# Kernel tuning notes

Measured on AMD Instinct MI355X. Metric: run time of the kernel, lower is better.

## Reference

```python
import jax, jax.numpy as jnp
import numpy as np

B, LQ, LF, NW, NFR, E, D, V = 4, 128, 64, 2, 8, 128, 128, 64


def _project(x, W, b):
    # torch Emb_Projection('linear'): Linear then zero-row mask
    y = x @ W + b
    m = 1.0 - jnp.all(y == 0, axis=-1, keepdims=True).astype(y.dtype)
    return y * m


def setup_inputs() -> dict:
    key = jax.random.key(0)
    ks = jax.random.split(key, 12)
    s = lambda k, shape, fan: jax.random.normal(k, shape, jnp.float32) / np.sqrt(fan)
    return {
        "query": jax.random.normal(ks[0], (B, LQ, E), jnp.float32),
        "fragment": jax.random.normal(ks[1], (B, NW, NFR, LF, E), jnp.float32),
        "query_mask": jnp.ones((B, LQ), jnp.float32),
        "fragment_mask": jnp.ones((B, NW, NFR, LF), jnp.float32),
        # learned params (stored [in, out]; torch Linear is x @ W.T with W [out,in])
        "proj_W": s(ks[2], (E, D), E),
        "proj_b": jnp.zeros((D,), jnp.float32),
        "self_att_W": s(ks[3], (NW, D), D),   # n_way Linear(D,1,bias=False)
        "q_att_W": s(ks[4], (D, V), D),
        "f_att_W": s(ks[5], (D, V), D),
        "qf_att_W": s(ks[6], (D, V), D),
        "gate_w": s(ks[7], (V,), V),          # value_gate: Linear(V,1,bias=False)
        "val_w": s(ks[8], (V,), V),           # value_att:  Linear(V,1,bias=False)
    }


def reference(query, fragment, query_mask, fragment_mask, proj_W, proj_b,
              self_att_W, q_att_W, f_att_W, qf_att_W, gate_w, val_w):
    query = _project(query, proj_W, proj_b)          # [B,Lq,D]
    fragment = _project(fragment, proj_W, proj_b)    # [B,NW,NFR,Lf,D]

    # (1) fragment self-attention -> frag_code
    logits = jnp.einsum('bwfld,wd->bwfl', fragment, self_att_W)   # per-way Linear(D,1)
    e = jnp.exp(logits) * fragment_mask
    frag_self_att = e / (e.sum(-1, keepdims=True) + 1e-7)          # [B,NW,NFR,Lf]
    frag_code = (fragment * frag_self_att[..., None]).sum(-2)     # [B,NW,NFR,D]

    # (2) query-to-fragment attention
    frag_r = fragment.reshape(fragment.shape[0], -1, fragment.shape[-2], fragment.shape[-1])  # [B,NF,Lf,D]
    qr = query[:, None]                                            # [B,1,Lq,D]
    q_att = qr @ q_att_W                                           # [B,1,Lq,V]
    f_att = frag_r @ f_att_W                                       # [B,NF,Lf,V]
    # large broadcast product [B,NF,Lf,Lq,D] then project to V
    qf = (qr[:, :, None, :, :] * frag_r[:, :, :, None, :]) @ qf_att_W  # [B,NF,Lf,Lq,V]
    qf = q_att[:, :, None] + f_att[:, :, :, None] + qf
    qf = qf.max(axis=-3)                                           # max over Lf -> [B,NF,Lq,V]

    qf_gate = jax.nn.sigmoid(qf @ gate_w) * query_mask[:, None]    # [B,NF,Lq]
    e2 = jnp.exp(qf @ val_w) * query_mask[:, None]
    qf_norm = e2 / (e2.sum(-1, keepdims=True) + 1e-7)              # [B,NF,Lq]

    query_code = (qr * qf_norm[..., None]).sum(axis=2)             # [B,NF,D]
    query_code = query_code.reshape(frag_code.shape)               # [B,NW,NFR,D]
    return frag_code, query_code, frag_self_att, qf_gate, query
```

## Files before the change

### kernel.cpp

```cpp
#include <hip/hip_runtime.h>
#include <hip/hip_bf16.h>

#define B_   4
#define LQ_  128
#define LF_  64
#define NW_  2
#define NFR_ 8
#define E_   128
#define D_   128
#define V_   64
#define NWF_ (NW_*NFR_)

using bf16 = __hip_bfloat16;
typedef unsigned short u16;
typedef unsigned int   u32;
typedef __attribute__((ext_vector_type(8))) short  bf16x8;
typedef __attribute__((ext_vector_type(2))) float  f32x2;
typedef __attribute__((ext_vector_type(4))) float  f32x4;
typedef __attribute__((ext_vector_type(4))) u32    u32x4;

#define WS_PWT   0
#define WS_QAT   8192
#define WS_W3T   12288
#define WS_WFT   16384
#define WS_E2    20480
#define WS_QPB   28672

#define OUT_FRAGCODE  0
#define OUT_QUERYCODE 8192
#define OUT_SELFATT   16384
#define OUT_QFGATE    20480
#define OUT_QUERY     28672

#define L_FP   0
#define L_QP   16384
#define L_FA   24576
#define L_QAT  33792
#define L_SAW  38400
#define L_ATT  38912
#define L_RED  39168
#define L_PM   41216
#define L_TOT  57600

__device__ __forceinline__ float us2f(u16 v) { return __uint_as_float((u32)v << 16); }
__device__ __forceinline__ float lo2f(u32 v) { return __uint_as_float(v << 16); }
__device__ __forceinline__ float hi2f(u32 v) { return __uint_as_float(v & 0xffff0000u); }
__device__ __forceinline__ u16 f2b_raw(float f) {
    u32 u = __float_as_uint(f);
    return (u16)((u + 0x7fffu + ((u >> 16) & 1u)) >> 16);
}
__device__ __forceinline__ u32 pk2(float hi, float lo) {
    return __builtin_amdgcn_perm(__float_as_uint(hi), __float_as_uint(lo), 0x07060302u);
}
template<bool BF> __device__ __forceinline__ float LD(const void* p, int i) {
    return BF ? us2f(((const u16*)p)[i]) : ((const float*)p)[i];
}
template<bool BF> __device__ __forceinline__ void ST(void* p, int i, float v) {
    if (BF) ((u16*)p)[i] = f2b_raw(v); else ((float*)p)[i] = v;
}
template<bool BF> __device__ __forceinline__ u16 LDB(const void* p, int i) {
    return BF ? ((const u16*)p)[i] : f2b_raw(((const float*)p)[i]);
}
__device__ __forceinline__ bool is_bf(const void* qmask) {
    return ((const u16*)qmask)[0] == 0x3F80u;
}
template<bool BF>
__device__ __forceinline__ bf16x8 loadA(const void* x, int row, int kt, int quad) {
    int off = row * 128 + kt * 32 + quad * 8;
    if (BF) return *(const bf16x8*)((const u16*)x + off);
    f32x4 a = *(const f32x4*)((const float*)x + off);
    f32x4 c = *(const f32x4*)((const float*)x + off + 4);
    u32x4 av;
    av.x = pk2(a.y, a.x); av.y = pk2(a.w, a.z);
    av.z = pk2(c.y, c.x); av.w = pk2(c.w, c.z);
    return __builtin_bit_cast(bf16x8, av);
}

template<bool BF>
__device__ __forceinline__ void prep_body(const void* src, u16* dst, u16* stg,
                                          int N, int k0)
{
    int t = threadIdx.x, st = N + 1, total = 32 * N;
    for (int i = t; i < total; i += 256) {
        int k = i / N, v = i % N;
        stg[k * st + v] = LDB<BF>(src, (k0 + k) * N + v);
    }
    __syncthreads();
    for (int j = t; j < total; j += 256) {
        int n = j >> 5, kk = j & 31;
        dst[n * 128 + k0 + kk] = stg[kk * st + n];
    }
}
__global__ __launch_bounds__(256) void k_prep(
    const void* projW, const void* qattW, const void* qfW, const void* fattW,
    const void* qmask, float* ws)
{
    __shared__ u16 stg[32 * 129];
    int mat = blockIdx.x >> 2, kq = blockIdx.x & 3;
    const void* src = (mat == 0) ? projW : (mat == 1) ? qattW : (mat == 2) ? qfW : fattW;
    u16* dst = (u16*)(ws + ((mat == 0) ? WS_PWT : (mat == 1) ? WS_QAT : (mat == 2) ? WS_W3T : WS_WFT));
    int N = (mat == 0) ? 128 : 64;
    if (is_bf(qmask)) prep_body<true >(src, dst, stg, N, kq * 32);
    else              prep_body<false>(src, dst, stg, N, kq * 32);
}

template<bool BF>
__device__ __forceinline__ void main_body(
    const void* query, const void* fragment, const void* qmask, const void* fmask,
    const void* projB, const void* saW, const void* gatew, const void* valw,
    float* ws, void* out, char* smem)
{
    u16*   s_fp  = (u16*)(smem + L_FP);
    u16*   s_qp  = (u16*)(smem + L_QP);
    u16*   s_fa  = (u16*)(smem + L_FA);
    u16*   s_qat = (u16*)(smem + L_QAT);
    float* s_saw = (float*)(smem + L_SAW);
    float* s_att = (float*)(smem + L_ATT);
    float* s_red = (float*)(smem + L_RED);
    u16*   s_pm  = (u16*)(smem + L_PM);

    int bx = blockIdx.x;
    int qt = bx >> 6, bwf = bx & 63, b = bwf >> 4;
    int t = threadIdx.x, lane = t & 63, w = t >> 6;
    int m = lane & 15, quad = lane >> 4;
    int sk = (m & 7) << 3;
    const u16* pwt = (const u16*)(ws + WS_PWT);
    const u16* qatw = (const u16*)(ws + WS_QAT);
    const u16* w3t = (const u16*)(ws + WS_W3T);
    const u16* wft = (const u16*)(ws + WS_WFT);
    bool do_fragatt = (qt == (bwf & 3));
    bool do_export  = ((bwf & 15) == 0);

    if (w < 4) {
        bf16x8 afr[4];
        #pragma unroll
        for (int kt = 0; kt < 4; ++kt)
            afr[kt] = loadA<BF>(fragment, bwf * 64 + w * 16 + m, kt, quad);
        #pragma unroll
        for (int nt = 0; nt < 8; ++nt) {
            int n = nt * 16 + m;
            float bv = LD<BF>(projB, n);
            f32x4 acc = (f32x4){bv, bv, bv, bv};
            #pragma unroll
            for (int kt = 0; kt < 4; ++kt) {
                bf16x8 bw = *(const bf16x8*)(pwt + n * 128 + kt * 32 + quad * 8);
                acc = __builtin_amdgcn_mfma_f32_16x16x32_bf16(afr[kt], bw, acc, 0, 0, 0);
            }
            #pragma unroll
            for (int rr = 0; rr < 4; ++rr) {
                int row = w * 16 + quad * 4 + rr;
                s_fp[row * 128 + (n ^ ((row & 7) << 3))] = f2b_raw(acc[rr]);
            }
        }
    } else if (w < 6) {
        int q0 = (w - 4) * 16;
        bf16x8 afq[4];
        #pragma unroll
        for (int kt = 0; kt < 4; ++kt)
            afq[kt] = loadA<BF>(query, b * 128 + qt * 32 + q0 + m, kt, quad);
        #pragma unroll
        for (int nt = 0; nt < 8; ++nt) {
            int n = nt * 16 + m;
            float bv = LD<BF>(projB, n);
            f32x4 acc = (f32x4){bv, bv, bv, bv};
            #pragma unroll
            for (int kt = 0; kt < 4; ++kt) {
                bf16x8 bw = *(const bf16x8*)(pwt + n * 128 + kt * 32 + quad * 8);
                acc = __builtin_amdgcn_mfma_f32_16x16x32_bf16(afq[kt], bw, acc, 0, 0, 0);
            }
            #pragma unroll
            for (int rr = 0; rr < 4; ++rr) {
                int row = q0 + quad * 4 + rr;
                s_qp[row * 128 + (n ^ ((row & 7) << 3))] = f2b_raw(acc[rr]);
            }
        }
    }
    __syncthreads();

    if (w < 4) {
        bf16x8 afa[4];
        #pragma unroll
        for (int kt = 0; kt < 4; ++kt)
            afa[kt] = *(const bf16x8*)&s_fp[(w * 16 + m) * 128 + ((kt * 32 + quad * 8) ^ sk)];
        #pragma unroll
        for (int vt = 0; vt < 4; ++vt) {
            f32x4 a0 = (f32x4){0.f, 0.f, 0.f, 0.f};
            #pragma unroll
            for (int kt = 0; kt < 4; ++kt) {
                bf16x8 wk = *(const bf16x8*)(wft + (vt * 16 + m) * 128 + kt * 32 + quad * 8);
                a0 = __builtin_amdgcn_mfma_f32_16x16x32_bf16(afa[kt], wk, a0, 0, 0, 0);
            }
            #pragma unroll
            for (int r = 0; r < 4; ++r)
                s_fa[(w * 16 + quad * 4 + r) * 72 + vt * 16 + m] = f2b_raw(a0[r]);
        }
    } else if (w < 6) {
        int q0 = (w - 4) * 16;
        bf16x8 aq[4];
        #pragma unroll
        for (int kt = 0; kt < 4; ++kt)
            aq[kt] = *(const bf16x8*)&s_qp[(q0 + m) * 128 + ((kt * 32 + quad * 8) ^ sk)];
        #pragma unroll
        for (int vt = 0; vt < 4; ++vt) {
            f32x4 a0 = (f32x4){0.f, 0.f, 0.f, 0.f};
            #pragma unroll
            for (int kt = 0; kt < 4; ++kt) {
                bf16x8 bk = *(const bf16x8*)(qatw + (vt * 16 + m) * 128 + kt * 32 + quad * 8);
                a0 = __builtin_amdgcn_mfma_f32_16x16x32_bf16(aq[kt], bk, a0, 0, 0, 0);
            }
            #pragma unroll
            for (int r = 0; r < 4; ++r)
                s_qat[(q0 + quad * 4 + r) * 72 + vt * 16 + m] = f2b_raw(a0[r]);
        }
    }
    __syncthreads();

    int qsub = w & 1, lq = w >> 1;
    bf16x8 w3f[4][4];
    #pragma unroll
    for (int vt = 0; vt < 4; ++vt)
        #pragma unroll
        for (int kt = 0; kt < 4; ++kt)
            w3f[vt][kt] = *(const bf16x8*)(w3t + (vt * 16 + m) * 128 + kt * 32 + quad * 8);
    f32x2 qp2[4][4];
    {
        #pragma unroll
        for (int kt = 0; kt < 4; ++kt) {
            bf16x8 aq2 = *(const bf16x8*)&s_qp[(qsub * 16 + m) * 128 + ((kt * 32 + quad * 8) ^ sk)];
            u32x4 uv = __builtin_bit_cast(u32x4, aq2);
            qp2[kt][0] = (f32x2){lo2f(uv.x), hi2f(uv.x)};
            qp2[kt][1] = (f32x2){lo2f(uv.y), hi2f(uv.y)};
            qp2[kt][2] = (f32x2){lo2f(uv.z), hi2f(uv.z)};
            qp2[kt][3] = (f32x2){lo2f(uv.w), hi2f(uv.w)};
        }
    }
    float mx[4][4];
    #pragma unroll
    for (int vt = 0; vt < 4; ++vt)
        #pragma unroll
        for (int r = 0; r < 4; ++r) mx[vt][r] = -1e30f;

    int lbase = lq * 16;
    #pragma unroll 2
    for (int li = 0; li < 16; ++li) {
        int l = lbase + li;
        int sw = (l & 7) << 3;
        bf16x8 af[4];
        #pragma unroll
        for (int kt = 0; kt < 4; ++kt) {
            u32x4 fv = *(const u32x4*)&s_fp[l * 128 + ((kt * 32 + quad * 8) ^ sw)];
            f32x2 p0 = qp2[kt][0] * (f32x2){lo2f(fv.x), hi2f(fv.x)};
            f32x2 p1 = qp2[kt][1] * (f32x2){lo2f(fv.y), hi2f(fv.y)};
            f32x2 p2 = qp2[kt][2] * (f32x2){lo2f(fv.z), hi2f(fv.z)};
            f32x2 p3 = qp2[kt][3] * (f32x2){lo2f(fv.w), hi2f(fv.w)};
            u32x4 av;
            av.x = pk2(p0.y, p0.x);
            av.y = pk2(p1.y, p1.x);
            av.z = pk2(p2.y, p2.x);
            av.w = pk2(p3.y, p3.x);
            af[kt] = __builtin_bit_cast(bf16x8, av);
        }
        #pragma unroll
        for (int vt = 0; vt < 4; ++vt) {
            float fa = us2f(s_fa[l * 72 + vt * 16 + m]);
            f32x4 acc = (f32x4){fa, fa, fa, fa};
            #pragma unroll
            for (int kt = 0; kt < 4; ++kt)
                acc = __builtin_amdgcn_mfma_f32_16x16x32_bf16(af[kt], w3f[vt][kt], acc, 0, 0, 0);
            #pragma unroll
            for (int r = 0; r < 4; ++r) mx[vt][r] = fmaxf(mx[vt][r], acc[r]);
        }
    }
    #pragma unroll
    for (int vt = 0; vt < 4; ++vt)
        #pragma unroll
        for (int r = 0; r < 4; ++r) {
            int q = qsub * 16 + quad * 4 + r;
            s_pm[(lq * 32 + q) * 64 + ((vt * 16 + m) ^ (((q >> 2) & 3) << 4))] = f2b_raw(mx[vt][r]);
        }
    __syncthreads();

    {
        int q = t >> 4, vg = t & 15;
        int gq = qt * 32 + q;
        int swq = ((q >> 2) & 3) << 4;
        float gp = 0.f, ep = 0.f;
        #pragma unroll
        for (int jj = 0; jj < 4; ++jj) {
            int v = vg * 4 + jj;
            int c = v ^ swq;
            float m01 = fmaxf(us2f(s_pm[q * 64 + c]),        us2f(s_pm[(32 + q) * 64 + c]));
            float m23 = fmaxf(us2f(s_pm[(64 + q) * 64 + c]), us2f(s_pm[(96 + q) * 64 + c]));
            float qf = fmaxf(m01, m23) + us2f(s_qat[q * 72 + v]);
            gp += qf * LD<BF>(gatew, v);
            ep += qf * LD<BF>(valw, v);
        }
        #pragma unroll
        for (int off = 1; off <= 8; off <<= 1) {
            gp += __shfl_xor(gp, off, 64);
            ep += __shfl_xor(ep, off, 64);
        }
        if (vg == 0) {
            float qm = LD<BF>(qmask, b * 128 + gq);
            float g = (1.0f / (1.0f + expf(-gp))) * qm;
            ST<BF>(out, OUT_QFGATE + bwf * LQ_ + gq, g);
            ws[WS_E2 + bwf * 128 + gq] = expf(ep) * qm;
        }
    }

    if (do_export) {
        u16* qpb = (u16*)(ws + WS_QPB);
        #pragma unroll
        for (int it = 0; it < 8; ++it) {
            int i = t + 512 * it;
            int row = i >> 7, col = i & 127;
            u16 raw = s_qp[row * 128 + (col ^ ((row & 7) << 3))];
            int gr = b * 128 + qt * 32 + row;
            ST<BF>(out, OUT_QUERY + gr * 128 + col, us2f(raw));
            qpb[gr * 128 + col] = raw;
        }
    }

    if (do_fragatt) {
        if (t < 128) s_saw[t] = LD<BF>(saW, ((bwf >> 3) & 1) * 128 + t);
        __syncthreads();
        {
            int l = t >> 3, j8 = t & 7;
            int swz = (l & 7) << 3;
            float p = 0.f;
            #pragma unroll
            for (int seg = 0; seg < 2; ++seg) {
                int koff = j8 * 16 + seg * 8;
                u32x4 fv = *(const u32x4*)&s_fp[l * 128 + (koff ^ swz)];
                const float* swp = &s_saw[koff];
                p += lo2f(fv.x) * swp[0] + hi2f(fv.x) * swp[1]
                   + lo2f(fv.y) * swp[2] + hi2f(fv.y) * swp[3]
                   + lo2f(fv.z) * swp[4] + hi2f(fv.z) * swp[5]
                   + lo2f(fv.w) * swp[6] + hi2f(fv.w) * swp[7];
            }
            p += __shfl_xor(p, 1, 64);
            p += __shfl_xor(p, 2, 64);
            p += __shfl_xor(p, 4, 64);
            if (j8 == 0) s_att[l] = expf(p) * LD<BF>(fmask, bwf * LF_ + l);
        }
        __syncthreads();
        if (t < 64) {
            float e = s_att[t], s = e;
            #pragma unroll
            for (int off = 1; off <= 32; off <<= 1) s += __shfl_xor(s, off, 64);
            float nrm = e / (s + 1e-7f);
            s_att[t] = nrm;
            ST<BF>(out, OUT_SELFATT + bwf * LF_ + t, nrm);
        }
        __syncthreads();
        {
            int d = t & 127, grp = t >> 7;
            float fc = 0.f;
            #pragma unroll
            for (int li2 = 0; li2 < 16; ++li2) {
                int l2 = grp * 16 + li2;
                fc += us2f(s_fp[l2 * 128 + (d ^ ((l2 & 7) << 3))]) * s_att[l2];
            }
            s_red[grp * 128 + d] = fc;
        }
        __syncthreads();
        if (t < 128)
            ST<BF>(out, OUT_FRAGCODE + bwf * D_ + t,
                   s_red[t] + s_red[128 + t] + s_red[256 + t] + s_red[384 + t]);
    }
}
__global__ __launch_bounds__(512, 2) void k_main(
    const void* query, const void* fragment, const void* qmask, const void* fmask,
    const void* projB, const void* saW, const void* gatew, const void* valw,
    float* ws, void* out)
{
    __shared__ char smem[L_TOT];
    if (is_bf(qmask))
        main_body<true >(query, fragment, qmask, fmask, projB, saW, gatew, valw, ws, out, smem);
    else
        main_body<false>(query, fragment, qmask, fmask, projB, saW, gatew, valw, ws, out, smem);
}

template<bool BF>
__device__ __forceinline__ void qcode_body(const float* ws, void* out,
                                           u16* s_q, float* s_n, float* s_part)
{
    int bwf = blockIdx.x, b = bwf >> 4, t = threadIdx.x;
    {
        const u32* src = (const u32*)((const u16*)(ws + WS_QPB) + (size_t)b * 16384);
        u32* dst = (u32*)s_q;
        #pragma unroll
        for (int it = 0; it < 64; ++it) dst[t + 128 * it] = src[t + 128 * it];
    }
    float e = ws[WS_E2 + bwf * 128 + t];
    float s = e;
    #pragma unroll
    for (int off = 1; off <= 32; off <<= 1) s += __shfl_xor(s, off, 64);
    if ((t & 63) == 0) s_part[t >> 6] = s;
    __syncthreads();
    float tot = s_part[0] + s_part[1] + 1e-7f;
    s_n[t] = e / tot;
    __syncthreads();
    float qc = 0.f;
    #pragma unroll 8
    for (int q = 0; q < 128; ++q)
        qc += us2f(s_q[q * 128 + t]) * s_n[q];
    ST<BF>(out, OUT_QUERYCODE + bwf * D_ + t, qc);
}
__global__ __launch_bounds__(128) void k_qcode(const void* qmask, const float* ws, void* out)
{
    __shared__ u16 s_q[128 * 128];
    __shared__ float s_n[128];
    __shared__ float s_part[2];
    if (is_bf(qmask)) qcode_body<true >(ws, out, s_q, s_n, s_part);
    else              qcode_body<false>(ws, out, s_q, s_n, s_part);
}

extern "C" void kernel_launch(void* const* d_in, const int* in_sizes, int n_in,
                              void* d_out, int out_size, void* d_ws, size_t ws_size,
                              hipStream_t stream)
{
    const void* query    = d_in[0];
    const void* fragment = d_in[1];
    const void* qmask    = d_in[2];
    const void* fmask    = d_in[3];
    const void* projW    = d_in[4];
    const void* projB    = d_in[5];
    const void* saW      = d_in[6];
    const void* qattW    = d_in[7];
    const void* fattW    = d_in[8];
    const void* qfW      = d_in[9];
    const void* gatew    = d_in[10];
    const void* valw     = d_in[11];
    float* ws = (float*)d_ws;

    hipLaunchKernelGGL(k_prep, dim3(16), dim3(256), 0, stream,
                       projW, qattW, qfW, fattW, qmask, ws);
    hipLaunchKernelGGL(k_main, dim3(256), dim3(512), 0, stream,
                       query, fragment, qmask, fmask, projB, saW, gatew, valw, ws, d_out);
    hipLaunchKernelGGL(k_qcode, dim3(B_ * NWF_), dim3(128), 0, stream,
                       qmask, ws, d_out);
}
```

Baseline: 109.1 us.

## Fuse prep, main and qcode kernels into one cooperative kernel with grid syncs

```diff
diff --git a/kernel.cpp b/kernel.cpp
--- a/kernel.cpp
+++ b/kernel.cpp
@@ -1,5 +1,8 @@
 #include <hip/hip_runtime.h>
 #include <hip/hip_bf16.h>
+#include <hip/hip_cooperative_groups.h>
+
+namespace cg = cooperative_groups;
 
 #define B_   4
 #define LQ_  128
@@ -41,6 +44,10 @@
 #define L_RED  39168
 #define L_PM   41216
 #define L_TOT  57600
+#define LQ_SQ    0
+#define LQ_SN    32768
+#define LQ_SP    33280
+#define LQ_SR    33536
 
 __device__ __forceinline__ float us2f(u16 v) { return __uint_as_float((u32)v << 16); }
 __device__ __forceinline__ float lo2f(u32 v) { return __uint_as_float(v << 16); }
@@ -81,27 +88,15 @@
                                           int N, int k0)
 {
     int t = threadIdx.x, st = N + 1, total = 32 * N;
-    for (int i = t; i < total; i += 256) {
+    for (int i = t; i < total; i += 512) {
         int k = i / N, v = i % N;
         stg[k * st + v] = LDB<BF>(src, (k0 + k) * N + v);
     }
     __syncthreads();
-    for (int j = t; j < total; j += 256) {
+    for (int j = t; j < total; j += 512) {
         int n = j >> 5, kk = j & 31;
         dst[n * 128 + k0 + kk] = stg[kk * st + n];
     }
-}
-__global__ __launch_bounds__(256) void k_prep(
-    const void* projW, const void* qattW, const void* qfW, const void* fattW,
-    const void* qmask, float* ws)
-{
-    __shared__ u16 stg[32 * 129];
-    int mat = blockIdx.x >> 2, kq = blockIdx.x & 3;
-    const void* src = (mat == 0) ? projW : (mat == 1) ? qattW : (mat == 2) ? qfW : fattW;
-    u16* dst = (u16*)(ws + ((mat == 0) ? WS_PWT : (mat == 1) ? WS_QAT : (mat == 2) ? WS_W3T : WS_WFT));
-    int N = (mat == 0) ? 128 : 64;
-    if (is_bf(qmask)) prep_body<true >(src, dst, stg, N, kq * 32);
-    else              prep_body<false>(src, dst, stg, N, kq * 32);
 }
 
 template<bool BF>
@@ -369,51 +364,88 @@
                    s_red[t] + s_red[128 + t] + s_red[256 + t] + s_red[384 + t]);
     }
 }
-__global__ __launch_bounds__(512, 2) void k_main(
-    const void* query, const void* fragment, const void* qmask, const void* fmask,
-    const void* projB, const void* saW, const void* gatew, const void* valw,
-    float* ws, void* out)
-{
-    __shared__ char smem[L_TOT];
-    if (is_bf(qmask))
-        main_body<true >(query, fragment, qmask, fmask, projB, saW, gatew, valw, ws, out, smem);
-    else
-        main_body<false>(query, fragment, qmask, fmask, projB, saW, gatew, valw, ws, out, smem);
-}
 
 template<bool BF>
-__device__ __forceinline__ void qcode_body(const float* ws, void* out,
-                                           u16* s_q, float* s_n, float* s_part)
-{
-    int bwf = blockIdx.x, b = bwf >> 4, t = threadIdx.x;
+__device__ __forceinline__ void qcode_body(int bwf, const float* ws, void* out,
+                                           char* smem)
+{
+    u16*   s_q    = (u16*)(smem + LQ_SQ);
+    float* s_n    = (float*)(smem + LQ_SN);
+    float* s_part = (float*)(smem + LQ_SP);
+    float* s_r4   = (float*)(smem + LQ_SR);
+    int b = bwf >> 4, t = threadIdx.x;
     {
         const u32* src = (const u32*)((const u16*)(ws + WS_QPB) + (size_t)b * 16384);
         u32* dst = (u32*)s_q;
         #pragma unroll
-        for (int it = 0; it < 64; ++it) dst[t + 128 * it] = src[t + 128 * it];
-    }
-    float e = ws[WS_E2 + bwf * 128 + t];
-    float s = e;
-    #pragma unroll
-    for (int off = 1; off <= 32; off <<= 1) s += __shfl_xor(s, off, 64);
-    if ((t & 63) == 0) s_part[t >> 6] = s;
-    __syncthreads();
-    float tot = s_part[0] + s_part[1] + 1e-7f;
-    s_n[t] = e / tot;
-    __syncthreads();
-    float qc = 0.f;
-    #pragma unroll 8
-    for (int q = 0; q < 128; ++q)
-        qc += us2f(s_q[q * 128 + t]) * s_n[q];
-    ST<BF>(out, OUT_QUERYCODE + bwf * D_ + t, qc);
-}
-__global__ __launch_bounds__(128) void k_qcode(const void* qmask, const float* ws, void* out)
-{
-    __shared__ u16 s_q[128 * 128];
-    __shared__ float s_n[128];
-    __shared__ float s_part[2];
-    if (is_bf(qmask)) qcode_body<true >(ws, out, s_q, s_n, s_part);
-    else              qcode_body<false>(ws, out, s_q, s_n, s_part);
+        for (int it = 0; it < 16; ++it) dst[t + 512 * it] = src[t + 512 * it];
+    }
+    float e = 0.f;
+    if (t < 128) {
+        e = ws[WS_E2 + bwf * 128 + t];
+        float s = e;
+        #pragma unroll
+        for (int off = 1; off <= 32; off <<= 1) s += __shfl_xor(s, off, 64);
+        if ((t & 63) == 0) s_part[t >> 6] = s;
+    }
+    __syncthreads();
+    if (t < 128) s_n[t] = e / (s_part[0] + s_part[1] + 1e-7f);
+    __syncthreads();
+    {
+        int d = t & 127, grp = t >> 7;
+        float qc = 0.f;
+        #pragma unroll 8
+        for (int qi = 0; qi < 32; ++qi) {
+            int q = grp * 32 + qi;
+            qc += us2f(s_q[q * 128 + d]) * s_n[q];
+        }
+        s_r4[grp * 128 + d] = qc;
+    }
+    __syncthreads();
+    if (t < 128)
+        ST<BF>(out, OUT_QUERYCODE + bwf * D_ + t,
+               s_r4[t] + s_r4[128 + t] + s_r4[256 + t] + s_r4[384 + t]);
+}
+
+template<bool BF>
+__device__ __forceinline__ void run_all(
+    const void* query, const void* fragment, const void* qmask, const void* fmask,
+    const void* projB, const void* saW, const void* gatew, const void* valw,
+    const void* projW, const void* qattW, const void* qfW, const void* fattW,
+    float* ws, void* out, char* smem)
+{
+    cg::grid_group grid = cg::this_grid();
+    int bx = blockIdx.x;
+
+    if ((bx & 15) == ((bx >> 4) & 7)) {
+        int pu = bx >> 4, mat = pu >> 2, kq = pu & 3;
+        const void* src = (mat == 0) ? projW : (mat == 1) ? qattW : (mat == 2) ? qfW : fattW;
+        u16* dst = (u16*)(ws + ((mat == 0) ? WS_PWT : (mat == 1) ? WS_QAT : (mat == 2) ? WS_W3T : WS_WFT));
+        int N = (mat == 0) ? 128 : 64;
+        prep_body<BF>(src, dst, (u16*)smem, N, kq * 32);
+    }
+    grid.sync();
+
+    main_body<BF>(query, fragment, qmask, fmask, projB, saW, gatew, valw, ws, out, smem);
+    grid.sync();
+
+    if ((bx & 3) == ((bx >> 2) & 3))
+        qcode_body<BF>(bx >> 2, ws, out, smem);
+}
+
+__global__ __launch_bounds__(512, 2) void k_all(
+    const void* query, const void* fragment, const void* qmask, const void* fmask,
+    const void* projB, const void* saW, const void* gatew, const void* valw,
+    const void* projW, const void* qattW, const void* qfW, const void* fattW,
+    float* ws, void* out)
+{
+    __shared__ __align__(16) char smem[L_TOT];
+    if (is_bf(qmask))
+        run_all<true >(query, fragment, qmask, fmask, projB, saW, gatew, valw,
+                       projW, qattW, qfW, fattW, ws, out, smem);
+    else
+        run_all<false>(query, fragment, qmask, fmask, projB, saW, gatew, valw,
+                       projW, qattW, qfW, fattW, ws, out, smem);
 }
 
 extern "C" void kernel_launch(void* const* d_in, const int* in_sizes, int n_in,
@@ -433,11 +465,13 @@
     const void* gatew    = d_in[10];
     const void* valw     = d_in[11];
     float* ws = (float*)d_ws;
-
-    hipLaunchKernelGGL(k_prep, dim3(16), dim3(256), 0, stream,
-                       projW, qattW, qfW, fattW, qmask, ws);
-    hipLaunchKernelGGL(k_main, dim3(256), dim3(512), 0, stream,
-                       query, fragment, qmask, fmask, projB, saW, gatew, valw, ws, d_out);
-    hipLaunchKernelGGL(k_qcode, dim3(B_ * NWF_), dim3(128), 0, stream,
-                       qmask, ws, d_out);
-}
+    void* out = d_out;
+
+    void* args[] = {
+        (void*)&query, (void*)&fragment, (void*)&qmask, (void*)&fmask,
+        (void*)&projB, (void*)&saW, (void*)&gatew, (void*)&valw,
+        (void*)&projW, (void*)&qattW, (void*)&qfW, (void*)&fattW,
+        (void*)&ws, (void*)&out
+    };
+    hipLaunchCooperativeKernel((void*)k_all, dim3(256), dim3(512), args, 0, stream);
+}
```

Result: slower. 174.7 us (+60.1%).

## Fuse prep and qcode kernels into single kernel with LDS-staged weights and last-block tail

Applied to the files above, without the earlier changes.

```diff
diff --git a/kernel.cpp b/kernel.cpp
--- a/kernel.cpp
+++ b/kernel.cpp
@@ -19,12 +19,9 @@
 typedef __attribute__((ext_vector_type(4))) float  f32x4;
 typedef __attribute__((ext_vector_type(4))) u32    u32x4;
 
-#define WS_PWT   0
-#define WS_QAT   8192
-#define WS_W3T   12288
-#define WS_WFT   16384
 #define WS_E2    20480
 #define WS_QPB   28672
+#define WS_CNT   61440
 
 #define OUT_FRAGCODE  0
 #define OUT_QUERYCODE 8192
@@ -40,7 +37,14 @@
 #define L_ATT  38912
 #define L_RED  39168
 #define L_PM   41216
-#define L_TOT  57600
+#define L_PWT  57600
+#define L_QATW 90368
+#define L_W3T  106752
+#define L_WFT  123136
+#define L_TOT  139520
+#define LT_SQ    0
+#define LT_SN    32768
+#define LT_PP    40960
 
 __device__ __forceinline__ float us2f(u16 v) { return __uint_as_float((u32)v << 16); }
 __device__ __forceinline__ float lo2f(u32 v) { return __uint_as_float(v << 16); }
@@ -77,37 +81,76 @@
 }
 
 template<bool BF>
-__device__ __forceinline__ void prep_body(const void* src, u16* dst, u16* stg,
-                                          int N, int k0)
+__device__ __forceinline__ void stage_one(const void* src, u16* dst, u16* stg,
+                                          int N, int st)
 {
-    int t = threadIdx.x, st = N + 1, total = 32 * N;
-    for (int i = t; i < total; i += 256) {
-        int k = i / N, v = i % N;
-        stg[k * st + v] = LDB<BF>(src, (k0 + k) * N + v);
-    }
-    __syncthreads();
-    for (int j = t; j < total; j += 256) {
-        int n = j >> 5, kk = j & 31;
-        dst[n * 128 + k0 + kk] = stg[kk * st + n];
-    }
-}
-__global__ __launch_bounds__(256) void k_prep(
-    const void* projW, const void* qattW, const void* qfW, const void* fattW,
-    const void* qmask, float* ws)
+    int t = threadIdx.x;
+    for (int i = t; i < 128 * N; i += 512) {
+        int k = (N == 128) ? (i >> 7) : (i >> 6);
+        int v = (N == 128) ? (i & 127) : (i & 63);
+        stg[k * st + v] = LDB<BF>(src, k * N + v);
+    }
+    __syncthreads();
+    for (int j = t; j < N * 128; j += 512) {
+        int n = j >> 7, kk = j & 127;
+        dst[n * 128 + (kk ^ ((n & 7) << 3))] = stg[kk * st + n];
+    }
+    __syncthreads();
+}
+
+template<bool BF>
+__device__ __forceinline__ void qcode_tail(int b, const float* ws, void* out,
+                                           char* smem)
 {
-    __shared__ u16 stg[32 * 129];
-    int mat = blockIdx.x >> 2, kq = blockIdx.x & 3;
-    const void* src = (mat == 0) ? projW : (mat == 1) ? qattW : (mat == 2) ? qfW : fattW;
-    u16* dst = (u16*)(ws + ((mat == 0) ? WS_PWT : (mat == 1) ? WS_QAT : (mat == 2) ? WS_W3T : WS_WFT));
-    int N = (mat == 0) ? 128 : 64;
-    if (is_bf(qmask)) prep_body<true >(src, dst, stg, N, kq * 32);
-    else              prep_body<false>(src, dst, stg, N, kq * 32);
+    u16*   s_q  = (u16*)(smem + LT_SQ);
+    float* s_n  = (float*)(smem + LT_SN);
+    float* s_pp = (float*)(smem + LT_PP);
+    int t = threadIdx.x, lane = t & 63, w = t >> 6;
+    {
+        const u32* src = (const u32*)((const u16*)(ws + WS_QPB) + (size_t)b * 16384);
+        u32* dst = (u32*)s_q;
+        #pragma unroll
+        for (int it = 0; it < 16; ++it) dst[t + 512 * it] = src[t + 512 * it];
+    }
+    #pragma unroll
+    for (int rr = 0; rr < 2; ++rr) {
+        int row = w * 2 + rr;
+        float e0 = ws[WS_E2 + (b * 16 + row) * 128 + lane];
+        float e1 = ws[WS_E2 + (b * 16 + row) * 128 + 64 + lane];
+        float s = e0 + e1;
+        #pragma unroll
+        for (int off = 1; off <= 32; off <<= 1) s += __shfl_xor(s, off, 64);
+        float inv = 1.0f / (s + 1e-7f);
+        s_n[row * 128 + lane]      = e0 * inv;
+        s_n[row * 128 + 64 + lane] = e1 * inv;
+    }
+    __syncthreads();
+    {
+        int d = t & 127, grp = t >> 7;
+        for (int bw2 = 0; bw2 < 16; ++bw2) {
+            float acc = 0.f;
+            #pragma unroll 8
+            for (int qi = 0; qi < 32; ++qi) {
+                int q = grp * 32 + qi;
+                acc += us2f(s_q[q * 128 + d]) * s_n[bw2 * 128 + q];
+            }
+            s_pp[(bw2 * 4 + grp) * 128 + d] = acc;
+        }
+    }
+    __syncthreads();
+    for (int idx = t; idx < 2048; idx += 512) {
+        int bw2 = idx >> 7, d = idx & 127;
+        float v = s_pp[(bw2 * 4 + 0) * 128 + d] + s_pp[(bw2 * 4 + 1) * 128 + d]
+                + s_pp[(bw2 * 4 + 2) * 128 + d] + s_pp[(bw2 * 4 + 3) * 128 + d];
+        ST<BF>(out, OUT_QUERYCODE + (b * 16 + bw2) * D_ + d, v);
+    }
 }
 
 template<bool BF>
 __device__ __forceinline__ void main_body(
     const void* query, const void* fragment, const void* qmask, const void* fmask,
     const void* projB, const void* saW, const void* gatew, const void* valw,
+    const void* projW, const void* qattW, const void* qfW, const void* fattW,
     float* ws, void* out, char* smem)
 {
     u16*   s_fp  = (u16*)(smem + L_FP);
@@ -118,18 +161,23 @@
     float* s_att = (float*)(smem + L_ATT);
     float* s_red = (float*)(smem + L_RED);
     u16*   s_pm  = (u16*)(smem + L_PM);
+    u16*   pwt   = (u16*)(smem + L_PWT);
+    u16*   qatw  = (u16*)(smem + L_QATW);
+    u16*   w3t   = (u16*)(smem + L_W3T);
+    u16*   wft   = (u16*)(smem + L_WFT);
 
     int bx = blockIdx.x;
     int qt = bx >> 6, bwf = bx & 63, b = bwf >> 4;
     int t = threadIdx.x, lane = t & 63, w = t >> 6;
     int m = lane & 15, quad = lane >> 4;
     int sk = (m & 7) << 3;
-    const u16* pwt = (const u16*)(ws + WS_PWT);
-    const u16* qatw = (const u16*)(ws + WS_QAT);
-    const u16* w3t = (const u16*)(ws + WS_W3T);
-    const u16* wft = (const u16*)(ws + WS_WFT);
     bool do_fragatt = (qt == (bwf & 3));
     bool do_export  = ((bwf & 15) == 0);
+
+    stage_one<BF>(projW, pwt,  (u16*)smem, 128, 129);
+    stage_one<BF>(qattW, qatw, (u16*)smem, 64, 65);
+    stage_one<BF>(qfW,   w3t,  (u16*)smem, 64, 65);
+    stage_one<BF>(fattW, wft,  (u16*)smem, 64, 65);
 
     if (w < 4) {
         bf16x8 afr[4];
@@ -143,7 +191,7 @@
             f32x4 acc = (f32x4){bv, bv, bv, bv};
             #pragma unroll
             for (int kt = 0; kt < 4; ++kt) {
-                bf16x8 bw = *(const bf16x8*)(pwt + n * 128 + kt * 32 + quad * 8);
+                bf16x8 bw = *(const bf16x8*)&pwt[n * 128 + ((kt * 32 + quad * 8) ^ sk)];
                 acc = __builtin_amdgcn_mfma_f32_16x16x32_bf16(afr[kt], bw, acc, 0, 0, 0);
             }
             #pragma unroll
@@ -165,7 +213,7 @@
             f32x4 acc = (f32x4){bv, bv, bv, bv};
             #pragma unroll
             for (int kt = 0; kt < 4; ++kt) {
-                bf16x8 bw = *(const bf16x8*)(pwt + n * 128 + kt * 32 + quad * 8);
+                bf16x8 bw = *(const bf16x8*)&pwt[n * 128 + ((kt * 32 + quad * 8) ^ sk)];
                 acc = __builtin_amdgcn_mfma_f32_16x16x32_bf16(afq[kt], bw, acc, 0, 0, 0);
             }
             #pragma unroll
@@ -187,7 +235,7 @@
             f32x4 a0 = (f32x4){0.f, 0.f, 0.f, 0.f};
             #pragma unroll
             for (int kt = 0; kt < 4; ++kt) {
-                bf16x8 wk = *(const bf16x8*)(wft + (vt * 16 + m) * 128 + kt * 32 + quad * 8);
+                bf16x8 wk = *(const bf16x8*)&wft[(vt * 16 + m) * 128 + ((kt * 32 + quad * 8) ^ sk)];
                 a0 = __builtin_amdgcn_mfma_f32_16x16x32_bf16(afa[kt], wk, a0, 0, 0, 0);
             }
             #pragma unroll
@@ -205,7 +253,7 @@
             f32x4 a0 = (f32x4){0.f, 0.f, 0.f, 0.f};
             #pragma unroll
             for (int kt = 0; kt < 4; ++kt) {
-                bf16x8 bk = *(const bf16x8*)(qatw + (vt * 16 + m) * 128 + kt * 32 + quad * 8);
+                bf16x8 bk = *(const bf16x8*)&qatw[(vt * 16 + m) * 128 + ((kt * 32 + quad * 8) ^ sk)];
                 a0 = __builtin_amdgcn_mfma_f32_16x16x32_bf16(aq[kt], bk, a0, 0, 0, 0);
             }
             #pragma unroll
@@ -221,7 +269,7 @@
     for (int vt = 0; vt < 4; ++vt)
         #pragma unroll
         for (int kt = 0; kt < 4; ++kt)
-            w3f[vt][kt] = *(const bf16x8*)(w3t + (vt * 16 + m) * 128 + kt * 32 + quad * 8);
+            w3f[vt][kt] = *(const bf16x8*)&w3t[(vt * 16 + m) * 128 + ((kt * 32 + quad * 8) ^ sk)];
     f32x2 qp2[4][4];
     {
         #pragma unroll
@@ -368,52 +416,36 @@
             ST<BF>(out, OUT_FRAGCODE + bwf * D_ + t,
                    s_red[t] + s_red[128 + t] + s_red[256 + t] + s_red[384 + t]);
     }
-}
-__global__ __launch_bounds__(512, 2) void k_main(
+
+    __threadfence();
+    __syncthreads();
+    if (t == 0) {
+        u32* cnt = (u32*)(ws + WS_CNT);
+        u32 old = __hip_atomic_fetch_add(&cnt[b], 1u, __ATOMIC_ACQ_REL,
+                                         __HIP_MEMORY_SCOPE_AGENT);
+        *(volatile int*)(smem + L_RED) = (old == 63u) ? 1 : 0;
+    }
+    __syncthreads();
+    int amlast = *(volatile int*)(smem + L_RED);
+    if (!amlast) return;
+    __threadfence();
+    __syncthreads();
+    qcode_tail<BF>(b, ws, out, smem);
+}
+
+__global__ __launch_bounds__(512, 2) void k_single(
     const void* query, const void* fragment, const void* qmask, const void* fmask,
     const void* projB, const void* saW, const void* gatew, const void* valw,
+    const void* projW, const void* qattW, const void* qfW, const void* fattW,
     float* ws, void* out)
 {
-    __shared__ char smem[L_TOT];
+    __shared__ __align__(16) char smem[L_TOT];
     if (is_bf(qmask))
-        main_body<true >(query, fragment, qmask, fmask, projB, saW, gatew, valw, ws, out, smem);
+        main_body<true >(query, fragment, qmask, fmask, projB, saW, gatew, valw,
+                         projW, qattW, qfW, fattW, ws, out, smem);
     else
-        main_body<false>(query, fragment, qmask, fmask, projB, saW, gatew, valw, ws, out, smem);
-}
-
-template<bool BF>
-__device__ __forceinline__ void qcode_body(const float* ws, void* out,
-                                           u16* s_q, float* s_n, float* s_part)
-{
-    int bwf = blockIdx.x, b = bwf >> 4, t = threadIdx.x;
-    {
-        const u32* src = (const u32*)((const u16*)(ws + WS_QPB) + (size_t)b * 16384);
-        u32* dst = (u32*)s_q;
-        #pragma unroll
-        for (int it = 0; it < 64; ++it) dst[t + 128 * it] = src[t + 128 * it];
-    }
-    float e = ws[WS_E2 + bwf * 128 + t];
-    float s = e;
-    #pragma unroll
-    for (int off = 1; off <= 32; off <<= 1) s += __shfl_xor(s, off, 64);
-    if ((t & 63) == 0) s_part[t >> 6] = s;
-    __syncthreads();
-    float tot = s_part[0] + s_part[1] + 1e-7f;
-    s_n[t] = e / tot;
-    __syncthreads();
-    float qc = 0.f;
-    #pragma unroll 8
-    for (int q = 0; q < 128; ++q)
-        qc += us2f(s_q[q * 128 + t]) * s_n[q];
-    ST<BF>(out, OUT_QUERYCODE + bwf * D_ + t, qc);
-}
-__global__ __launch_bounds__(128) void k_qcode(const void* qmask, const float* ws, void* out)
-{
-    __shared__ u16 s_q[128 * 128];
-    __shared__ float s_n[128];
-    __shared__ float s_part[2];
-    if (is_bf(qmask)) qcode_body<true >(ws, out, s_q, s_n, s_part);
-    else              qcode_body<false>(ws, out, s_q, s_n, s_part);
+        main_body<false>(query, fragment, qmask, fmask, projB, saW, gatew, valw,
+                         projW, qattW, qfW, fattW, ws, out, smem);
 }
 
 extern "C" void kernel_launch(void* const* d_in, const int* in_sizes, int n_in,
@@ -434,10 +466,9 @@
     const void* valw     = d_in[11];
     float* ws = (float*)d_ws;
 
-    hipLaunchKernelGGL(k_prep, dim3(16), dim3(256), 0, stream,
-                       projW, qattW, qfW, fattW, qmask, ws);
-    hipLaunchKernelGGL(k_main, dim3(256), dim3(512), 0, stream,
-                       query, fragment, qmask, fmask, projB, saW, gatew, valw, ws, d_out);
-    hipLaunchKernelGGL(k_qcode, dim3(B_ * NWF_), dim3(128), 0, stream,
-                       qmask, ws, d_out);
-}
+    hipMemsetAsync((char*)d_ws + WS_CNT * sizeof(float), 0, 4 * sizeof(u32), stream);
+
+    hipLaunchKernelGGL(k_single, dim3(256), dim3(512), 0, stream,
+                       query, fragment, qmask, fmask, projB, saW, gatew, valw,
+                       projW, qattW, qfW, fattW, ws, d_out);
+}
```

New measurement: 157.0 us. 1.44x slower.
